# Kernel optimization log

Hardware: AMD Instinct MI355X
Metric: run time of the kernel (lower is better)

Reference implementation:

```python
import jax, jax.numpy as jnp
import numpy as np

N, D, K, H, G = 200000, 256, 128, 4, 1024  # nodes, emb_dim, hidden, heads, graphs


def setup_inputs() -> dict:
    key = jax.random.key(0)
    k0, k1, k2, k3 = jax.random.split(key, 4)
    node_features = jax.random.normal(k0, (N, D), jnp.float32)
    segment_ids = jnp.sort(jax.random.randint(k1, (N,), 0, G)).astype(jnp.int32)
    W1 = jax.random.normal(k2, (H, D, K), jnp.float32) / np.float32(np.sqrt(D))
    b1 = jnp.zeros((H, K), jnp.float32)
    W2 = jax.random.normal(k3, (H, K), jnp.float32) / np.float32(np.sqrt(K))
    b2 = jnp.zeros((H,), jnp.float32)
    return {"node_features": node_features, "segment_ids": segment_ids,
            "num_graphs": G, "W1": W1, "b1": b1, "W2": W2, "b2": b2}


def _segment_softmax(scores, seg, num_segments):
    # scores: [N, H]; numerically-stable softmax within each graph segment, per head
    m = jax.ops.segment_max(scores, seg, num_segments=num_segments)  # [G, H]
    e = jnp.exp(scores - m[seg])
    s = jax.ops.segment_sum(e, seg, num_segments=num_segments)  # [G, H]
    return e / s[seg]


def reference(node_features, segment_ids, num_graphs, W1, b1, W2, b2):
    # Per-head MLP score for all heads at once: [N, H]
    h = jax.nn.relu(jnp.einsum('nd,hdk->nhk', node_features, W1) + b1)
    scores = jnp.einsum('nhk,hk->nh', h, W2) + b2
    # dgl.softmax_nodes per head == segment softmax over graph ids
    attn = _segment_softmax(scores, segment_ids, num_graphs)  # [N, H]
    # combine_type == 'mean': mean_h segment_sum(attn_h * x)
    # == segment_sum(mean_h(attn_h) * x) since the sum is linear in attn.
    avg_attn = attn.mean(axis=1)  # [N]
    weighted = avg_attn[:, None] * node_features  # [N, D]
    return jax.ops.segment_sum(weighted, segment_ids, num_segments=num_graphs)  # [G, D]
```

## Files before the change

kernel.cpp:

```cpp
#include <hip/hip_runtime.h>
#include <hip/hip_bf16.h>

typedef unsigned short u16;
typedef __attribute__((ext_vector_type(8))) __bf16 bf16x8;
typedef __attribute__((ext_vector_type(8))) u16 u16x8;
typedef __attribute__((ext_vector_type(4))) float f32x4;

__device__ __forceinline__ u16 f2bf(float f) {
    unsigned u = __float_as_uint(f);
    u += 0x7fffu + ((u >> 16) & 1u);
    return (u16)(u >> 16);
}

__device__ __forceinline__ void gl_lds16(const void* g, void* l) {
    __builtin_amdgcn_global_load_lds(
        (const __attribute__((address_space(1))) void*)g,
        (__attribute__((address_space(3))) void*)l, 16, 0, 0);
}

__global__ __launch_bounds__(256) void transpose_w1(const float* __restrict__ W1,
                                                    u16* __restrict__ W1T) {
    __shared__ u16 tile[64][132];
    const int t = threadIdx.x;
    const int h = blockIdx.x >> 2;
    const int dt = blockIdx.x & 3;
#pragma unroll
    for (int j = 0; j < 8; ++j) {
        int idx = j * 256 + t;
        int r = idx >> 5;
        int kq = idx & 31;
        float4 v = *reinterpret_cast<const float4*>(
            W1 + ((size_t)h * 256 + dt * 64 + r) * 128 + kq * 4);
        ushort4 o;
        o.x = f2bf(v.x); o.y = f2bf(v.y); o.z = f2bf(v.z); o.w = f2bf(v.w);
        *reinterpret_cast<ushort4*>(&tile[r][kq * 4]) = o;
    }
    __syncthreads();
#pragma unroll
    for (int j = 0; j < 4; ++j) {
        int idx = j * 256 + t;
        int k = idx >> 3;
        int c8 = idx & 7;
        u16x8 o;
#pragma unroll
        for (int e = 0; e < 8; ++e) o[e] = tile[c8 * 8 + e][k];
        *reinterpret_cast<u16x8*>(W1T + ((size_t)h * 128 + k) * 256 + dt * 64 + c8 * 8) = o;
    }
}

__global__ __launch_bounds__(256, 2) void score_kernel(
        const float* __restrict__ x, const u16* __restrict__ W1T,
        const float* __restrict__ b1, const float* __restrict__ W2,
        const float* __restrict__ b2, float* __restrict__ scores, int N) {
    __shared__ u16 xb[16384];
    __shared__ u16 sA[16384];

    const int t = threadIdx.x;
    const int wave = t >> 6;
    const int lane = t & 63;
    const int l15 = lane & 15;
    const int quad = lane >> 4;
    const int n0 = blockIdx.x * 64;

    {
        const int nrow = wave * 16 + (lane >> 2);
        const int koff = (lane & 3) * 8;
        int nn = n0 + nrow; if (nn >= N) nn = N - 1;
        const float* src = x + (size_t)nn * 256 + koff;
        float4 v[16];
#pragma unroll
        for (int i = 0; i < 8; ++i) {
            v[2 * i]     = *reinterpret_cast<const float4*>(src + i * 32);
            v[2 * i + 1] = *reinterpret_cast<const float4*>(src + i * 32 + 4);
        }
#pragma unroll
        for (int i = 0; i < 8; ++i) {
            u16x8 o;
            o[0] = f2bf(v[2*i].x);   o[1] = f2bf(v[2*i].y);
            o[2] = f2bf(v[2*i].z);   o[3] = f2bf(v[2*i].w);
            o[4] = f2bf(v[2*i+1].x); o[5] = f2bf(v[2*i+1].y);
            o[6] = f2bf(v[2*i+1].z); o[7] = f2bf(v[2*i+1].w);
            *reinterpret_cast<u16x8*>(&xb[(i * 256 + t) * 8]) = o;
        }
    }

    const int arr = (lane >> 2);
    const int akc = (lane & 3) * 8;
    auto stageA = [&](int ks) {
        const int k0 = ks * 32;
#pragma unroll
        for (int j = 0; j < 8; ++j) {
            int fr = wave * 8 + j;
            const u16* g = W1T + (size_t)(fr * 16 + arr) * 256 + k0 + akc;
            gl_lds16(g, &sA[(size_t)fr * 512]);
        }
    };

    f32x4 acc[8][4] = {};
    stageA(0);
    __syncthreads();

    for (int ks = 0; ks < 8; ++ks) {
        bf16x8 a[8], b[4];
#pragma unroll
        for (int fr = 0; fr < 8; ++fr)
            a[fr] = *reinterpret_cast<const bf16x8*>(
                &sA[((wave * 8 + fr) * 64 + l15 * 4 + quad) * 8]);
#pragma unroll
        for (int nf = 0; nf < 4; ++nf)
            b[nf] = *reinterpret_cast<const bf16x8*>(
                &xb[((ks * 4 + nf) * 64 + l15 * 4 + quad) * 8]);
        __syncthreads();
        if (ks < 7) stageA(ks + 1);
#pragma unroll
        for (int fr = 0; fr < 8; ++fr)
#pragma unroll
            for (int nf = 0; nf < 4; ++nf)
                acc[fr][nf] = __builtin_amdgcn_mfma_f32_16x16x32_bf16(
                    a[fr], b[nf], acc[fr][nf], 0, 0, 0);
        __syncthreads();
    }

    const int h = wave;
    float4 b1v[8], w2v[8];
#pragma unroll
    for (int fr = 0; fr < 8; ++fr) {
        int rb = h * 128 + fr * 16 + quad * 4;
        b1v[fr] = *reinterpret_cast<const float4*>(b1 + rb);
        w2v[fr] = *reinterpret_cast<const float4*>(W2 + rb);
    }
    const float b2v = b2[h];
#pragma unroll
    for (int nf = 0; nf < 4; ++nf) {
        float p = 0.f;
#pragma unroll
        for (int fr = 0; fr < 8; ++fr) {
            f32x4 c = acc[fr][nf];
            p += fmaxf(c[0] + b1v[fr].x, 0.f) * w2v[fr].x
               + fmaxf(c[1] + b1v[fr].y, 0.f) * w2v[fr].y
               + fmaxf(c[2] + b1v[fr].z, 0.f) * w2v[fr].z
               + fmaxf(c[3] + b1v[fr].w, 0.f) * w2v[fr].w;
        }
        p += __shfl_xor(p, 16, 64);
        p += __shfl_xor(p, 32, 64);
        int n = n0 + nf * 16 + lane;
        if (lane < 16 && n < N)
            scores[(size_t)n * 4 + h] = p + b2v;
    }
}

__device__ __forceinline__ int lower_bound(const int* __restrict__ a, int n, int v) {
    int lo = 0, hi = n;
    while (lo < hi) {
        int mid = (lo + hi) >> 1;
        if (a[mid] < v) lo = mid + 1; else hi = mid;
    }
    return lo;
}

__global__ __launch_bounds__(256) void segstat_kernel(
        const float4* __restrict__ scores4, const int* __restrict__ seg,
        float4* __restrict__ mOut, float4* __restrict__ isOut, int N) {
    __shared__ float4 redm[4];
    __shared__ float4 reds[4];
    const int g = blockIdx.x;
    const int t = threadIdx.x;
    const int start = lower_bound(seg, N, g);
    const int end = lower_bound(seg, N, g + 1);

    float4 mx = make_float4(-3.4e38f, -3.4e38f, -3.4e38f, -3.4e38f);
    for (int i = start + t; i < end; i += 256) {
        float4 s = scores4[i];
        mx.x = fmaxf(mx.x, s.x); mx.y = fmaxf(mx.y, s.y);
        mx.z = fmaxf(mx.z, s.z); mx.w = fmaxf(mx.w, s.w);
    }
#pragma unroll
    for (int off = 1; off < 64; off <<= 1) {
        mx.x = fmaxf(mx.x, __shfl_xor(mx.x, off, 64));
        mx.y = fmaxf(mx.y, __shfl_xor(mx.y, off, 64));
        mx.z = fmaxf(mx.z, __shfl_xor(mx.z, off, 64));
        mx.w = fmaxf(mx.w, __shfl_xor(mx.w, off, 64));
    }
    if ((t & 63) == 0) redm[t >> 6] = mx;
    __syncthreads();
    mx = redm[0];
#pragma unroll
    for (int w = 1; w < 4; ++w) {
        mx.x = fmaxf(mx.x, redm[w].x); mx.y = fmaxf(mx.y, redm[w].y);
        mx.z = fmaxf(mx.z, redm[w].z); mx.w = fmaxf(mx.w, redm[w].w);
    }

    float4 sm = make_float4(0.f, 0.f, 0.f, 0.f);
    for (int i = start + t; i < end; i += 256) {
        float4 s = scores4[i];
        sm.x += expf(s.x - mx.x); sm.y += expf(s.y - mx.y);
        sm.z += expf(s.z - mx.z); sm.w += expf(s.w - mx.w);
    }
#pragma unroll
    for (int off = 1; off < 64; off <<= 1) {
        sm.x += __shfl_xor(sm.x, off, 64);
        sm.y += __shfl_xor(sm.y, off, 64);
        sm.z += __shfl_xor(sm.z, off, 64);
        sm.w += __shfl_xor(sm.w, off, 64);
    }
    if ((t & 63) == 0) reds[t >> 6] = sm;
    __syncthreads();
    if (t == 0) {
        float4 tot = reds[0];
        for (int w = 1; w < 4; ++w) {
            tot.x += reds[w].x; tot.y += reds[w].y;
            tot.z += reds[w].z; tot.w += reds[w].w;
        }
        bool nonempty = end > start;
        float4 m_out = nonempty ? mx : make_float4(0.f, 0.f, 0.f, 0.f);
        float4 is;
        is.x = (nonempty && tot.x > 0.f) ? 1.f / tot.x : 0.f;
        is.y = (nonempty && tot.y > 0.f) ? 1.f / tot.y : 0.f;
        is.z = (nonempty && tot.z > 0.f) ? 1.f / tot.z : 0.f;
        is.w = (nonempty && tot.w > 0.f) ? 1.f / tot.w : 0.f;
        mOut[g] = m_out;
        isOut[g] = is;
    }
}

__global__ __launch_bounds__(256) void wsum_kernel(
        const float* __restrict__ x, const float4* __restrict__ scores4,
        const int* __restrict__ seg, const float4* __restrict__ mArr,
        const float4* __restrict__ isArr, float* __restrict__ out, int N) {
    __shared__ float wl[64];
    __shared__ int gl[64];
    __shared__ unsigned long long bmask_s;
    const int t = threadIdx.x;
    const int n0 = blockIdx.x * 64;
    const int cnt = min(64, N - n0);

    if (t < 64) {
        int g = -1;
        float w = 0.f;
        bool bnd = false;
        if (t < cnt) {
            int n = n0 + t;
            g = seg[n];
            float4 s = scores4[n];
            float4 m = mArr[g];
            float4 is = isArr[g];
            w = 0.25f * (expf(s.x - m.x) * is.x + expf(s.y - m.y) * is.y +
                         expf(s.z - m.z) * is.z + expf(s.w - m.w) * is.w);
            bnd = (t > 0) && (g != seg[n - 1]);
        }
        wl[t] = w;
        gl[t] = g;
        unsigned long long bm = __ballot(bnd);
        if (t == 0) bmask_s = bm;
    }
    __syncthreads();
    const unsigned long long bmask = bmask_s;

    int rs = 0;
    while (rs < cnt) {
        unsigned long long mm = (rs < 63) ? (bmask & ((~0ULL) << (rs + 1))) : 0ULL;
        int re = mm ? (__ffsll((long long)mm) - 1) : cnt;
        if (re > cnt) re = cnt;
        float acc = 0.f;
        int i = rs;
        for (; i + 8 <= re; i += 8) {
            float xv[8];
#pragma unroll
            for (int j = 0; j < 8; ++j)
                xv[j] = x[(size_t)(n0 + i + j) * 256 + t];
#pragma unroll
            for (int j = 0; j < 8; ++j) acc += wl[i + j] * xv[j];
        }
        for (; i < re; ++i) acc += wl[i] * x[(size_t)(n0 + i) * 256 + t];
        atomicAdd(&out[(size_t)gl[rs] * 256 + t], acc);
        rs = re;
    }
}

extern "C" void kernel_launch(void* const* d_in, const int* in_sizes, int n_in,
                              void* d_out, int out_size, void* d_ws, size_t ws_size,
                              hipStream_t stream) {
    const float* x  = (const float*)d_in[0];
    const int* seg  = (const int*)d_in[1];
    const float* W1 = (const float*)d_in[3];
    const float* b1 = (const float*)d_in[4];
    const float* W2 = (const float*)d_in[5];
    const float* b2 = (const float*)d_in[6];
    float* out = (float*)d_out;

    const int N = in_sizes[0] / 256;
    const int G = 1024;

    char* ws = (char*)d_ws;
    float* scores = (float*)ws;
    u16* W1T      = (u16*)(ws + (size_t)N * 16);
    float* mArr   = (float*)(ws + (size_t)N * 16 + 262144);
    float* isArr  = mArr + (size_t)G * 4;

    hipMemsetAsync(d_out, 0, (size_t)G * 256 * sizeof(float), stream);
    transpose_w1<<<16, 256, 0, stream>>>(W1, W1T);
    score_kernel<<<(N + 63) / 64, 256, 0, stream>>>(x, W1T, b1, W2, b2, scores, N);
    segstat_kernel<<<G, 256, 0, stream>>>((const float4*)scores, seg,
                                          (float4*)mArr, (float4*)isArr, N);
    wsum_kernel<<<(N + 63) / 64, 256, 0, stream>>>(x, (const float4*)scores, seg,
                                                   (const float4*)mArr,
                                                   (const float4*)isArr, out, N);
}
```

Baseline: 384.9 us.

## Load W1T fragments directly into registers and swizzle x tile in LDS

Replaces the LDS staging of W1T (global_load_lds plus per-step barriers) with direct global-to-register loads of each wave's A fragments, double-buffered across k-steps. The x tile in LDS is rewritten with an XOR-swizzled layout so the MFMA B-fragment reads avoid bank conflicts, and only one barrier remains after the x conversion. This cuts LDS traffic and synchronisation in the main loop. In exchange it raises register pressure from the two A buffers and relies on L2/cache hits for the repeated W1T reads.

```diff
diff --git a/kernel.cpp b/kernel.cpp
--- a/kernel.cpp
+++ b/kernel.cpp
@@ -10,12 +10,6 @@
     unsigned u = __float_as_uint(f);
     u += 0x7fffu + ((u >> 16) & 1u);
     return (u16)(u >> 16);
-}
-
-__device__ __forceinline__ void gl_lds16(const void* g, void* l) {
-    __builtin_amdgcn_global_load_lds(
-        (const __attribute__((address_space(1))) void*)g,
-        (__attribute__((address_space(3))) void*)l, 16, 0, 0);
 }
 
 __global__ __launch_bounds__(256) void transpose_w1(const float* __restrict__ W1,
@@ -53,7 +47,6 @@
         const float* __restrict__ b1, const float* __restrict__ W2,
         const float* __restrict__ b2, float* __restrict__ scores, int N) {
     __shared__ u16 xb[16384];
-    __shared__ u16 sA[16384];
 
     const int t = threadIdx.x;
     const int wave = t >> 6;
@@ -62,11 +55,21 @@
     const int quad = lane >> 4;
     const int n0 = blockIdx.x * 64;
 
+    const u16* aptr = W1T + ((size_t)wave * 128 + l15) * 256 + quad * 8;
+
+    bf16x8 a0[8], a1[8];
+#pragma unroll
+    for (int j = 0; j < 8; ++j)
+        a0[j] = *reinterpret_cast<const bf16x8*>(aptr + j * 4096);
+
     {
         const int nrow = wave * 16 + (lane >> 2);
         const int koff = (lane & 3) * 8;
         int nn = n0 + nrow; if (nn >= N) nn = N - 1;
         const float* src = x + (size_t)nn * 256 + koff;
+        const int l_t = ((lane & 3) << 4) | (lane >> 2);
+        const int q   = l_t ^ ((l_t >> 4) << 1);
+        u16* dst = xb + (size_t)wave * 512 + q * 8;
         float4 v[16];
 #pragma unroll
         for (int i = 0; i < 8; ++i) {
@@ -80,45 +83,35 @@
             o[2] = f2bf(v[2*i].z);   o[3] = f2bf(v[2*i].w);
             o[4] = f2bf(v[2*i+1].x); o[5] = f2bf(v[2*i+1].y);
             o[6] = f2bf(v[2*i+1].z); o[7] = f2bf(v[2*i+1].w);
-            *reinterpret_cast<u16x8*>(&xb[(i * 256 + t) * 8]) = o;
-        }
-    }
-
-    const int arr = (lane >> 2);
-    const int akc = (lane & 3) * 8;
-    auto stageA = [&](int ks) {
-        const int k0 = ks * 32;
-#pragma unroll
-        for (int j = 0; j < 8; ++j) {
-            int fr = wave * 8 + j;
-            const u16* g = W1T + (size_t)(fr * 16 + arr) * 256 + k0 + akc;
-            gl_lds16(g, &sA[(size_t)fr * 512]);
-        }
-    };
+            *reinterpret_cast<u16x8*>(dst + i * 2048) = o;
+        }
+    }
+
+    const int qr = lane ^ ((lane >> 4) << 1);
+    const u16* xrd = xb + qr * 8;
+
+    __syncthreads();
 
     f32x4 acc[8][4] = {};
-    stageA(0);
-    __syncthreads();
-
+#pragma unroll
     for (int ks = 0; ks < 8; ++ks) {
-        bf16x8 a[8], b[4];
-#pragma unroll
-        for (int fr = 0; fr < 8; ++fr)
-            a[fr] = *reinterpret_cast<const bf16x8*>(
-                &sA[((wave * 8 + fr) * 64 + l15 * 4 + quad) * 8]);
+        auto& a  = (ks & 1) ? a1 : a0;
+        auto& an = (ks & 1) ? a0 : a1;
+        bf16x8 b[4];
 #pragma unroll
         for (int nf = 0; nf < 4; ++nf)
-            b[nf] = *reinterpret_cast<const bf16x8*>(
-                &xb[((ks * 4 + nf) * 64 + l15 * 4 + quad) * 8]);
-        __syncthreads();
-        if (ks < 7) stageA(ks + 1);
+            b[nf] = *reinterpret_cast<const bf16x8*>(xrd + (ks * 4 + nf) * 512);
+        if (ks < 7) {
+#pragma unroll
+            for (int j = 0; j < 8; ++j)
+                an[j] = *reinterpret_cast<const bf16x8*>(aptr + j * 4096 + (ks + 1) * 32);
+        }
 #pragma unroll
         for (int fr = 0; fr < 8; ++fr)
 #pragma unroll
             for (int nf = 0; nf < 4; ++nf)
                 acc[fr][nf] = __builtin_amdgcn_mfma_f32_16x16x32_bf16(
                     a[fr], b[nf], acc[fr][nf], 0, 0, 0);
-        __syncthreads();
     }
 
     const int h = wave;
```

Measured after the change: 436.5 us. 13.4% more time.
